# Optimization experiments

Measured on AMD Instinct MI355X. Metric: run time of the kernel, lower is better.

The kernel has to match this reference:

```python
import jax, jax.numpy as jnp
import numpy as np

DECAY = 0.6
GAIN = 0.4


def _layernorm(x, g, b, eps=1e-5):
    m = x.mean(-1, keepdims=True)
    v = x.var(-1, keepdims=True)
    return (x - m) * jax.lax.rsqrt(v + eps) * g + b


def _ema_scan(x, axis, reverse=False):
    # linear recurrence state = 0.6*state + 0.4*x as an associative scan
    a = jnp.full_like(x, DECAY)
    b = GAIN * x
    def comb(c1, c2):
        a1, b1 = c1
        a2, b2 = c2
        return a1 * a2, a2 * b1 + b2
    _, y = jax.lax.associative_scan(comb, (a, b), axis=axis, reverse=reverse)
    return y


def setup_inputs() -> dict:
    key = jax.random.key(0)
    B, H, W, D = 16, 64, 64, 384
    inner = 2 * D
    hidden = 4 * D
    ks = jax.random.split(key, 12)
    s = 0.02
    return {
        "x": jax.random.normal(ks[0], (B, H, W, D), jnp.float32),
        "n1_g": jnp.ones((D,), jnp.float32),
        "n1_b": jnp.zeros((D,), jnp.float32),
        "w_in": s * jax.random.normal(ks[1], (D, inner), jnp.float32),
        "b_in": jnp.zeros((inner,), jnp.float32),
        "k_conv": s * jax.random.normal(ks[2], (3, 3, 1, inner), jnp.float32),  # depthwise HWIO
        "on_g": jnp.ones((inner,), jnp.float32),
        "on_b": jnp.zeros((inner,), jnp.float32),
        "w_out": s * jax.random.normal(ks[3], (inner, D), jnp.float32),
        "b_out": jnp.zeros((D,), jnp.float32),
        "n2_g": jnp.ones((D,), jnp.float32),
        "n2_b": jnp.zeros((D,), jnp.float32),
        "w1": s * jax.random.normal(ks[4], (D, hidden), jnp.float32),
        "b1": jnp.zeros((hidden,), jnp.float32),
        "w2": s * jax.random.normal(ks[5], (hidden, D), jnp.float32),
        "b2": jnp.zeros((D,), jnp.float32),
    }


def reference(x, n1_g, n1_b, w_in, b_in, k_conv, on_g, on_b, w_out, b_out,
              n2_g, n2_b, w1, b1, w2, b2):
    inner = w_in.shape[1]
    # --- LegacyScan2DOperator branch ---
    h = _layernorm(x, n1_g, n1_b)
    p = h @ w_in + b_in  # [B,H,W,inner]
    local = jax.lax.conv_general_dilated(
        p, k_conv, window_strides=(1, 1), padding="SAME",
        dimension_numbers=("NHWC", "HWIO", "NHWC"),
        feature_group_count=inner)
    lr = _ema_scan(local, axis=2)                 # left->right over W
    rl = _ema_scan(local, axis=2, reverse=True)   # right->left
    tb = _ema_scan(local, axis=1)                 # top->bottom over H
    bt = _ema_scan(local, axis=1, reverse=True)   # bottom->top
    mixed = 0.25 * (lr + rl + tb + bt) + local
    mixed = _layernorm(mixed, on_g, on_b)
    x = x + (mixed @ w_out + b_out)
    # --- MLP branch ---
    h2 = _layernorm(x, n2_g, n2_b)
    m = jax.nn.gelu(h2 @ w1 + b1, approximate=False) @ w2 + b2
    return x + m
```

## Files before the change

kernel.cpp:

```cpp
#include <hip/hip_runtime.h>
#include <math.h>


typedef __attribute__((ext_vector_type(8))) short bf16x8;
typedef __attribute__((ext_vector_type(4))) float f32x4;

#define T_TOKENS 65536
#define DMODEL 384
#define DINNER 768
#define DHIDDEN 1536

__device__ __forceinline__ float bf2f(unsigned short u) {
  unsigned int x = ((unsigned int)u) << 16;
  return __builtin_bit_cast(float, x);
}
__device__ __forceinline__ unsigned short f2bf(float f) {
  unsigned int x = __builtin_bit_cast(unsigned int, f);
  x += 0x7fffu + ((x >> 16) & 1u);
  return (unsigned short)(x >> 16);
}
__device__ __forceinline__ void unpack2(unsigned int u, float& lo, float& hi) {
  lo = __builtin_bit_cast(float, u << 16);
  hi = __builtin_bit_cast(float, u & 0xffff0000u);
}
__device__ __forceinline__ unsigned int pack2(float lo, float hi) {
  return (unsigned int)f2bf(lo) | ((unsigned int)f2bf(hi) << 16);
}
__device__ __forceinline__ unsigned int pack2t(float lo, float hi) {
  return (__builtin_bit_cast(unsigned int, lo) >> 16) |
         (__builtin_bit_cast(unsigned int, hi) & 0xffff0000u);
}

__device__ __forceinline__ void gload16(const void* g, void* l) {
  __builtin_amdgcn_global_load_lds(
      (const __attribute__((address_space(1))) void*)g,
      (__attribute__((address_space(3))) void*)l, 16, 0, 0);
}

__device__ __forceinline__ void wprep_tile(const float* __restrict__ in,
                                           unsigned short* __restrict__ out,
                                           int K, int N, int k0, int n0,
                                           int tid, float t[32][33]) {
  const int a = tid & 31, b8 = tid >> 5;
#pragma unroll
  for (int i = 0; i < 4; i++)
    t[b8 + 8 * i][a] = in[(size_t)(k0 + b8 + 8 * i) * N + n0 + a];
  __syncthreads();
#pragma unroll
  for (int i = 0; i < 4; i++)
    out[(size_t)(n0 + b8 + 8 * i) * K + k0 + a] = f2bf(t[a][b8 + 8 * i]);
}

__global__ __launch_bounds__(256) void ln1_wprep_kernel(
    const float* __restrict__ in, const float* __restrict__ g,
    const float* __restrict__ b, unsigned short* __restrict__ out,
    const float* __restrict__ win, unsigned short* __restrict__ wTin) {
  __shared__ float t[32][33];
  if (blockIdx.x >= 16384) {
    const int id = blockIdx.x - 16384;
    wprep_tile(win, wTin, DMODEL, DINNER, (id % 12) * 32, (id / 12) * 32,
               threadIdx.x, t);
    return;
  }
  const int tok = blockIdx.x * 4 + (threadIdx.x >> 6);
  const int lane = threadIdx.x & 63;
  const float2* row = (const float2*)(in + (size_t)tok * 384);
  float2 v[3];
  float s = 0.f, ss = 0.f;
#pragma unroll
  for (int k = 0; k < 3; k++) {
    v[k] = row[lane + 64 * k];
    s += v[k].x + v[k].y;
    ss += v[k].x * v[k].x + v[k].y * v[k].y;
  }
#pragma unroll
  for (int off = 32; off > 0; off >>= 1) {
    s += __shfl_xor(s, off);
    ss += __shfl_xor(ss, off);
  }
  const float m = s * (1.0f / 384.0f);
  const float r = rsqrtf(ss * (1.0f / 384.0f) - m * m + 1e-5f);
  unsigned int* op = (unsigned int*)(out + (size_t)tok * 384);
#pragma unroll
  for (int k = 0; k < 3; k++) {
    const int c = lane + 64 * k;
    const float2 gg = ((const float2*)g)[c];
    const float2 bb = ((const float2*)b)[c];
    op[c] = pack2((v[k].x - m) * r * gg.x + bb.x, (v[k].y - m) * r * gg.y + bb.y);
  }
}

__global__ __launch_bounds__(256) void ln_fused_bf16_384(
    const unsigned short* __restrict__ in, const float* __restrict__ g,
    const float* __restrict__ b, unsigned short* __restrict__ out) {
  const int tok = blockIdx.x * 4 + (threadIdx.x >> 6);
  const int lane = threadIdx.x & 63;
  const unsigned int* row = (const unsigned int*)(in + (size_t)tok * 384);
  unsigned int u[3];
  float e[3][2];
  float s = 0.f, ss = 0.f;
#pragma unroll
  for (int k = 0; k < 3; k++) {
    u[k] = row[lane + 64 * k];
    unpack2(u[k], e[k][0], e[k][1]);
    s += e[k][0] + e[k][1];
    ss += e[k][0] * e[k][0] + e[k][1] * e[k][1];
  }
#pragma unroll
  for (int off = 32; off > 0; off >>= 1) {
    s += __shfl_xor(s, off);
    ss += __shfl_xor(ss, off);
  }
  const float m = s * (1.0f / 384.0f);
  const float r = rsqrtf(ss * (1.0f / 384.0f) - m * m + 1e-5f);
  unsigned int* op = (unsigned int*)(out + (size_t)tok * 384);
#pragma unroll
  for (int k = 0; k < 3; k++) {
    const int c = lane + 64 * k;
    const float2 gg = ((const float2*)g)[c];
    const float2 bb = ((const float2*)b)[c];
    op[c] = pack2((e[k][0] - m) * r * gg.x + bb.x,
                  (e[k][1] - m) * r * gg.y + bb.y);
  }
}

__global__ __launch_bounds__(256) void ln_bundle_768(
    const uint2* __restrict__ mixed, const float* __restrict__ g,
    const float* __restrict__ b, uint2* __restrict__ out) {
  const int tid = threadIdx.x;
  const int tk = tid >> 2, j = tid & 3;
  const int token = blockIdx.x * 64 + tk;
  const int bb_ = token >> 12, posb = token & 4095;
  const size_t slab = (size_t)bb_ * 4096 + posb;
  float s = 0.f, ss = 0.f;
#pragma unroll 1
  for (int cg = j; cg < 192; cg += 4) {
    const uint2 v = mixed[((size_t)cg * 16) * 4096 + slab];
    float e0, e1, e2, e3;
    unpack2(v.x, e0, e1);
    unpack2(v.y, e2, e3);
    s += (e0 + e1) + (e2 + e3);
    ss += e0 * e0 + e1 * e1 + e2 * e2 + e3 * e3;
  }
  s += __shfl_xor(s, 1); ss += __shfl_xor(ss, 1);
  s += __shfl_xor(s, 2); ss += __shfl_xor(ss, 2);
  const float m = s * (1.0f / 768.0f);
  const float r = rsqrtf(ss * (1.0f / 768.0f) - m * m + 1e-5f);
  const size_t tokbase = (size_t)token * 192;
#pragma unroll 1
  for (int cg = j; cg < 192; cg += 4) {
    const uint2 v = mixed[((size_t)cg * 16) * 4096 + slab];
    const float4 gg = ((const float4*)g)[cg];
    const float4 bb4 = ((const float4*)b)[cg];
    float e0, e1, e2, e3;
    unpack2(v.x, e0, e1);
    unpack2(v.y, e2, e3);
    uint2 o;
    o.x = pack2((e0 - m) * r * gg.x + bb4.x, (e1 - m) * r * gg.y + bb4.y);
    o.y = pack2((e2 - m) * r * gg.z + bb4.z, (e3 - m) * r * gg.w + bb4.w);
    out[tokbase + cg] = o;
  }
}

__global__ __launch_bounds__(256) void wprep3_kernel(
    const float* __restrict__ wout, unsigned short* __restrict__ wToutp,
    const float* __restrict__ w1, unsigned short* __restrict__ wT1p,
    const float* __restrict__ w2, unsigned short* __restrict__ wT2p) {
  __shared__ float t[32][33];
  int id = blockIdx.x;
  if (id < 288) {
    wprep_tile(wout, wToutp, 768, 384, (id / 12) * 32, (id % 12) * 32,
               threadIdx.x, t);
  } else if (id < 864) {
    id -= 288;
    wprep_tile(w1, wT1p, 384, 1536, (id / 48) * 32, (id % 48) * 32,
               threadIdx.x, t);
  } else {
    id -= 864;
    wprep_tile(w2, wT2p, 1536, 384, (id / 12) * 32, (id % 12) * 32,
               threadIdx.x, t);
  }
}

template <int EPI>
__global__ __launch_bounds__(256, 4) void gemm_bt_kernel(
    const unsigned short* __restrict__ A, int lda,
    const unsigned short* __restrict__ Bt, int ldb, int KT,
    const float* __restrict__ bias, const void* __restrict__ res,
    void* __restrict__ C, int ldc, int nby) {
  __shared__ unsigned short smem[16640];
  char* const smc = (char*)smem;

  const int tid = threadIdx.x;
  const int w = tid >> 6, lane = tid & 63;
  const int cpx = gridDim.x >> 3;
  const int g = blockIdx.x;
  const int sw = (g & 7) * cpx + (g >> 3);
  const int bx = sw / nby, by = sw - bx * nby;
  const int tok0 = bx << 7, n0 = by << 7;

  const int wm = w >> 1, wn = w & 1;
  const int lrow = lane & 15, kgrp = lane >> 4;

  const int lr4 = lane >> 2;
  const int r0 = (w * 2 + 0) * 16 + lr4;
  const int r1 = (w * 2 + 1) * 16 + lr4;
  const int c0 = ((lane & 3) ^ ((r0 >> 1) & 3)) << 3;
  const int c1 = ((lane & 3) ^ ((r1 >> 1) & 3)) << 3;
  const unsigned short* A0 = A + (size_t)(tok0 + r0) * lda + c0;
  const unsigned short* A1p = A + (size_t)(tok0 + r1) * lda + c1;
  const unsigned short* B0 = Bt + (size_t)(n0 + r0) * ldb + c0;
  const unsigned short* B1 = Bt + (size_t)(n0 + r1) * ldb + c1;
  const int d0 = (w * 2 + 0) * 1024;
  const int d1 = (w * 2 + 1) * 1024;

  f32x4 acc[4][4];
#pragma unroll
  for (int i = 0; i < 4; i++)
#pragma unroll
    for (int j = 0; j < 4; j++) {
      f32x4 z = {0.f, 0.f, 0.f, 0.f};
      acc[i][j] = z;
    }

  const int nt = KT >> 5;
  gload16(A0, smc + d0);
  gload16(A1p, smc + d1);
  gload16(B0, smc + 16384 + d0);
  gload16(B1, smc + 16384 + d1);
  __syncthreads();

  int buf = 0;
  for (int t = 0; t < nt; t++) {
    if (t + 1 < nt) {
      const int kt = (t + 1) << 5;
      const int bo = (buf ^ 1) * 8192;
      gload16(A0 + kt, smc + bo + d0);
      gload16(A1p + kt, smc + bo + d1);
      gload16(B0 + kt, smc + 16384 + bo + d0);
      gload16(B1 + kt, smc + 16384 + bo + d1);
    }
    const int bo = buf * 8192;
    bf16x8 af[4], bf_[4];
#pragma unroll
    for (int f = 0; f < 4; f++) {
      const int ra = wm * 64 + f * 16 + lrow;
      const int rb = wn * 64 + f * 16 + lrow;
      af[f] = *(const bf16x8*)(smc + bo + ra * 64 +
                               ((kgrp ^ ((ra >> 1) & 3)) << 4));
      bf_[f] = *(const bf16x8*)(smc + 16384 + bo + rb * 64 +
                                ((kgrp ^ ((rb >> 1) & 3)) << 4));
    }
#pragma unroll
    for (int mf = 0; mf < 4; mf++)
#pragma unroll
      for (int nf = 0; nf < 4; nf++)
        acc[mf][nf] = __builtin_amdgcn_mfma_f32_16x16x32_bf16(
            af[mf], bf_[nf], acc[mf][nf], 0, 0, 0);
    __syncthreads();
    buf ^= 1;
  }

  if constexpr (EPI == 3) {
#pragma unroll
    for (int mf = 0; mf < 4; mf++)
#pragma unroll
      for (int nf = 0; nf < 4; nf++) {
        const int cl = wn * 64 + nf * 16 + lrow;
        const float bv = bias[n0 + cl];
#pragma unroll
        for (int r = 0; r < 4; r++) {
          const int tl = wm * 64 + mf * 16 + kgrp * 4 + r;
          smem[(cl >> 2) * 520 + tl * 4 + (cl & 3)] =
              f2bf(acc[mf][nf][r] + bv);
        }
      }
    __syncthreads();
    const int bb_ = tok0 >> 12, pos0 = tok0 & 4095, cg0 = n0 >> 2;
    uint2* Cb = (uint2*)C;
#pragma unroll
    for (int e = 0; e < 16; e++) {
      const int lin = e * 256 + tid;
      const int cgl = lin >> 7, pp = lin & 127;
      const uint2 v = *(const uint2*)&smem[cgl * 520 + pp * 4];
      Cb[((size_t)(cg0 + cgl) * 16 + bb_) * 4096 + pos0 + pp] = v;
    }
  } else {
#pragma unroll
    for (int mf = 0; mf < 4; mf++) {
#pragma unroll
      for (int nf = 0; nf < 4; nf++) {
        const int gcol = n0 + wn * 64 + nf * 16 + lrow;
        const float bv = bias ? bias[gcol] : 0.0f;
#pragma unroll
        for (int r = 0; r < 4; r++) {
          const int grow = tok0 + wm * 64 + mf * 16 + kgrp * 4 + r;
          float v = acc[mf][nf][r] + bv;
          const size_t idx = (size_t)grow * ldc + gcol;
          if constexpr (EPI == 4) {
            ((unsigned short*)C)[idx] = f2bf(v + ((const float*)res)[idx]);
          } else if constexpr (EPI == 5) {
            ((float*)C)[idx] = v + bf2f(((const unsigned short*)res)[idx]);
          } else {
            const float z = 1.5957691216057308f * (v + 0.044715f * v * v * v);
            const float gl = v / (1.0f + __expf(-z));
            ((unsigned short*)C)[idx] = f2bf(gl);
          }
        }
      }
    }
  }
}

__device__ __forceinline__ void ema_seg_f(const unsigned int vals[16],
                                          const int seg, float rl[16],
                                          float rh[16]) {
  const float A16 = 2.8211099e-4f;
  const float A32 = 7.9586611e-8f;
  float a, bv, t;
  float za = 0.f, zb = 0.f;
#pragma unroll
  for (int j = 0; j < 16; j++) {
    unpack2(vals[j], a, bv);
    za = 0.6f * za + 0.4f * a;
    zb = 0.6f * zb + 0.4f * bv;
  }
  t = __shfl_up(za, 1); if (seg >= 1) za += A16 * t;
  t = __shfl_up(zb, 1); if (seg >= 1) zb += A16 * t;
  t = __shfl_up(za, 2); if (seg >= 2) za += A32 * t;
  t = __shfl_up(zb, 2); if (seg >= 2) zb += A32 * t;
  float yfa = __shfl_up(za, 1), yfb = __shfl_up(zb, 1);
  if (seg == 0) { yfa = 0.f; yfb = 0.f; }
  float ua = 0.f, ub = 0.f;
#pragma unroll
  for (int j = 15; j >= 0; j--) {
    unpack2(vals[j], a, bv);
    ua = 0.6f * ua + 0.4f * a;
    ub = 0.6f * ub + 0.4f * bv;
  }
  t = __shfl_down(ua, 1); if (seg <= 2) ua += A16 * t;
  t = __shfl_down(ub, 1); if (seg <= 2) ub += A16 * t;
  t = __shfl_down(ua, 2); if (seg <= 1) ua += A32 * t;
  t = __shfl_down(ub, 2); if (seg <= 1) ub += A32 * t;
  float zba = __shfl_down(ua, 1), zbb = __shfl_down(ub, 1);
  if (seg == 3) { zba = 0.f; zbb = 0.f; }
  float fa = yfa, fb = yfb;
#pragma unroll
  for (int j = 0; j < 16; j++) {
    unpack2(vals[j], a, bv);
    fa = 0.6f * fa + 0.4f * a;
    fb = 0.6f * fb + 0.4f * bv;
    rl[j] = fa;
    rh[j] = fb;
  }
  float ga = zba, gb = zbb;
#pragma unroll
  for (int j = 15; j >= 0; j--) {
    unpack2(vals[j], a, bv);
    ga = 0.6f * ga + 0.4f * a;
    gb = 0.6f * gb + 0.4f * bv;
    rl[j] = 0.25f * (rl[j] + ga);
    rh[j] = 0.25f * (rh[j] + gb);
  }
}

__global__ __launch_bounds__(512) void conv_scan_kernel(
    const uint2* __restrict__ p, const float* __restrict__ kconv,
    uint2* __restrict__ mixed) {
  __shared__ unsigned int inp[2][64][65];
  __shared__ unsigned int loc[2][64][65];
  __shared__ float klds[36];
  const int tid = threadIdx.x;
  const int c = blockIdx.x;
  const int b = blockIdx.y;
  const uint2* pb = p + ((size_t)c * 16 + b) * 4096;

  if (tid < 36) klds[tid] = kconv[(tid >> 2) * DINNER + c * 4 + (tid & 3)];

#pragma unroll
  for (int i = 0; i < 8; i++) {
    const int pos = tid + 512 * i;
    const int h = pos >> 6, w = pos & 63;
    const uint2 pv = pb[pos];
    inp[0][h][w] = pv.x;
    inp[1][h][w] = pv.y;
  }
  __syncthreads();

#pragma unroll 2
  for (int i = 0; i < 8; i++) {
    const int pos = tid + 512 * i;
    const int h = pos >> 6, w = pos & 63;
    float a0 = 0.f, a1 = 0.f, a2 = 0.f, a3 = 0.f;
#pragma unroll
    for (int dh = 0; dh < 3; dh++) {
      const int hh = h + dh - 1;
      const bool vh = (unsigned)hh < 64u;
      const int hcl = min(max(hh, 0), 63);
#pragma unroll
      for (int dw = 0; dw < 3; dw++) {
        const int ww = w + dw - 1;
        const bool vv = vh && ((unsigned)ww < 64u);
        const int wcl = min(max(ww, 0), 63);
        unsigned int ux = inp[0][hcl][wcl];
        unsigned int uy = inp[1][hcl][wcl];
        if (!vv) { ux = 0; uy = 0; }
        const int t = dh * 3 + dw;
        float lo, hi;
        unpack2(ux, lo, hi);
        a0 += lo * klds[t * 4 + 0];
        a1 += hi * klds[t * 4 + 1];
        unpack2(uy, lo, hi);
        a2 += lo * klds[t * 4 + 2];
        a3 += hi * klds[t * 4 + 3];
      }
    }
    loc[0][h][w] = pack2t(a0, a1);
    loc[1][h][w] = pack2t(a2, a3);
  }
  __syncthreads();

  const int seg = tid & 3;
  const int ax = (tid >> 2) & 63;
  const int cp = tid >> 8;
  const int j0 = seg * 16;

  float hcl_[16], hch_[16];
  {
    unsigned int vals[16];
#pragma unroll
    for (int j = 0; j < 16; j++) vals[j] = loc[cp][j0 + j][ax];
    ema_seg_f(vals, seg, hcl_, hch_);
  }
  __syncthreads();

  {
    unsigned int vals[16];
    float wl[16], wh[16];
#pragma unroll
    for (int j = 0; j < 16; j++) vals[j] = loc[cp][ax][j0 + j];
    ema_seg_f(vals, seg, wl, wh);
#pragma unroll
    for (int j = 0; j < 16; j++) {
      float a, bv;
      unpack2(vals[j], a, bv);
      loc[cp][ax][j0 + j] = pack2t(a + wl[j], bv + wh[j]);
    }
  }
  __syncthreads();

#pragma unroll
  for (int j = 0; j < 16; j++) {
    float a, bv;
    unpack2(loc[cp][j0 + j][ax], a, bv);
    loc[cp][j0 + j][ax] = pack2t(a + hcl_[j], bv + hch_[j]);
  }
  __syncthreads();

  uint2* mb = mixed + ((size_t)c * 16 + b) * 4096;
#pragma unroll
  for (int i = 0; i < 8; i++) {
    const int pos = tid + 512 * i;
    const int h = pos >> 6, w = pos & 63;
    uint2 st;
    st.x = loc[0][h][w];
    st.y = loc[1][h][w];
    mb[pos] = st;
  }
}

extern "C" void kernel_launch(void* const* d_in, const int* in_sizes, int n_in,
                              void* d_out, int out_size, void* d_ws,
                              size_t ws_size, hipStream_t stream) {
  const float* x = (const float*)d_in[0];
  const float* n1_g = (const float*)d_in[1];
  const float* n1_b = (const float*)d_in[2];
  const float* w_in = (const float*)d_in[3];
  const float* b_in = (const float*)d_in[4];
  const float* k_conv = (const float*)d_in[5];
  const float* on_g = (const float*)d_in[6];
  const float* on_b = (const float*)d_in[7];
  const float* w_out = (const float*)d_in[8];
  const float* b_out = (const float*)d_in[9];
  const float* n2_g = (const float*)d_in[10];
  const float* n2_b = (const float*)d_in[11];
  const float* w1 = (const float*)d_in[12];
  const float* b1 = (const float*)d_in[13];
  const float* w2 = (const float*)d_in[14];
  const float* b2 = (const float*)d_in[15];

  const size_t MB = 1024 * 1024;
  char* ws = (char*)d_ws;
  unsigned short* R1 = (unsigned short*)(ws + 3 * MB / 2);
  unsigned short* R2 = (unsigned short*)(ws + 3 * MB / 2 + 96 * MB);

  unsigned short* A1 = R2;
  unsigned short* wTin = R2 + (48 * MB) / 2;
  unsigned short* p = R1;
  unsigned short* A2 = R2;
  unsigned short* x2b = R1;
  unsigned short* wT1 = R1 + (48 * MB) / 2;
  unsigned short* wT2 = wT1 + (size_t)1536 * 384;
  unsigned short* wTout = wT2 + (size_t)384 * 1536;
  unsigned short* gb = R2;

  float* out = (float*)d_out;
  unsigned short* A3 = (unsigned short*)out + (48 * MB) / 2;
  dim3 b256(256);

  ln1_wprep_kernel<<<16384 + 288, b256, 0, stream>>>(x, n1_g, n1_b, A1, w_in,
                                                     wTin);
  gemm_bt_kernel<3><<<3072, b256, 0, stream>>>(A1, DMODEL, wTin, DMODEL, DMODEL,
                                               b_in, nullptr, p, DINNER, 6);
  conv_scan_kernel<<<dim3(192, 16), dim3(512), 0, stream>>>(
      (const uint2*)p, k_conv, (uint2*)p);
  ln_bundle_768<<<1024, b256, 0, stream>>>((const uint2*)p, on_g, on_b,
                                           (uint2*)A2);
  wprep3_kernel<<<1440, b256, 0, stream>>>(w_out, wTout, w1, wT1, w2, wT2);
  gemm_bt_kernel<4><<<1536, b256, 0, stream>>>(A2, DINNER, wTout, DINNER,
                                               DINNER, b_out, x, x2b, DMODEL,
                                               3);
  ln_fused_bf16_384<<<T_TOKENS / 4, b256, 0, stream>>>(x2b, n2_g, n2_b, A3);
  for (int hh = 0; hh < 2; hh++) {
    const size_t toff = (size_t)hh * 32768;
    gemm_bt_kernel<2><<<3072, b256, 0, stream>>>(
        A3 + toff * DMODEL, DMODEL, wT1, DMODEL, DMODEL, b1, nullptr, gb,
        DHIDDEN, 12);
    gemm_bt_kernel<5><<<768, b256, 0, stream>>>(
        gb, DHIDDEN, wT2, DHIDDEN, DHIDDEN, b2, x2b + toff * DMODEL,
        out + toff * DMODEL, DMODEL, 3);
  }
}
```

Baseline: 621.8 us.

## Triple-buffer GEMM shared-memory tiles with a two-stage prefetch

The GEMM main loop moves from double to triple buffering in shared memory. Global-to-LDS loads for tile t+2 are issued after a vmcnt-based wait and one barrier per iteration, replacing the trailing __syncthreads. This is meant to hide more memory latency and drop one barrier per k-step. In exchange, LDS use grows to 48 KB per block and launch bounds drop from 4 to 3 blocks per CU, so fewer waves are resident.

```diff
diff --git a/kernel.cpp b/kernel.cpp
--- a/kernel.cpp
+++ b/kernel.cpp
@@ -183,13 +183,14 @@
 }
 
 template <int EPI>
-__global__ __launch_bounds__(256, 4) void gemm_bt_kernel(
+__global__ __launch_bounds__(256, 3) void gemm_bt_kernel(
     const unsigned short* __restrict__ A, int lda,
     const unsigned short* __restrict__ Bt, int ldb, int KT,
     const float* __restrict__ bias, const void* __restrict__ res,
     void* __restrict__ C, int ldc, int nby) {
-  __shared__ unsigned short smem[16640];
+  __shared__ unsigned short smem[24576];
   char* const smc = (char*)smem;
+  const int BOFF = 24576;
 
   const int tid = threadIdx.x;
   const int w = tid >> 6, lane = tid & 63;
@@ -224,21 +225,34 @@
     }
 
   const int nt = KT >> 5;
-  gload16(A0, smc + d0);
-  gload16(A1p, smc + d1);
-  gload16(B0, smc + 16384 + d0);
-  gload16(B1, smc + 16384 + d1);
-  __syncthreads();
+  {
+    gload16(A0, smc + d0);
+    gload16(A1p, smc + d1);
+    gload16(B0, smc + BOFF + d0);
+    gload16(B1, smc + BOFF + d1);
+    const int kt = 32;
+    gload16(A0 + kt, smc + 8192 + d0);
+    gload16(A1p + kt, smc + 8192 + d1);
+    gload16(B0 + kt, smc + BOFF + 8192 + d0);
+    gload16(B1 + kt, smc + BOFF + 8192 + d1);
+  }
 
   int buf = 0;
   for (int t = 0; t < nt; t++) {
     if (t + 1 < nt) {
-      const int kt = (t + 1) << 5;
-      const int bo = (buf ^ 1) * 8192;
-      gload16(A0 + kt, smc + bo + d0);
-      gload16(A1p + kt, smc + bo + d1);
-      gload16(B0 + kt, smc + 16384 + bo + d0);
-      gload16(B1 + kt, smc + 16384 + bo + d1);
+      asm volatile("s_waitcnt vmcnt(4)" ::: "memory");
+    } else {
+      asm volatile("s_waitcnt vmcnt(0)" ::: "memory");
+    }
+    __builtin_amdgcn_s_barrier();
+    __builtin_amdgcn_sched_barrier(0);
+    if (t + 2 < nt) {
+      const int kt = (t + 2) << 5;
+      const int so = ((t + 2) % 3) * 8192;
+      gload16(A0 + kt, smc + so + d0);
+      gload16(A1p + kt, smc + so + d1);
+      gload16(B0 + kt, smc + BOFF + so + d0);
+      gload16(B1 + kt, smc + BOFF + so + d1);
     }
     const int bo = buf * 8192;
     bf16x8 af[4], bf_[4];
@@ -248,7 +262,7 @@
       const int rb = wn * 64 + f * 16 + lrow;
       af[f] = *(const bf16x8*)(smc + bo + ra * 64 +
                                ((kgrp ^ ((ra >> 1) & 3)) << 4));
-      bf_[f] = *(const bf16x8*)(smc + 16384 + bo + rb * 64 +
+      bf_[f] = *(const bf16x8*)(smc + BOFF + bo + rb * 64 +
                                 ((kgrp ^ ((rb >> 1) & 3)) << 4));
     }
 #pragma unroll
@@ -257,11 +271,11 @@
       for (int nf = 0; nf < 4; nf++)
         acc[mf][nf] = __builtin_amdgcn_mfma_f32_16x16x32_bf16(
             af[mf], bf_[nf], acc[mf][nf], 0, 0, 0);
+    buf = (buf + 1) % 3;
+  }
+
+  if constexpr (EPI == 3) {
     __syncthreads();
-    buf ^= 1;
-  }
-
-  if constexpr (EPI == 3) {
 #pragma unroll
     for (int mf = 0; mf < 4; mf++)
 #pragma unroll
```

Result: no change. 610.9 us, median of 2 (-1.7%).
